# Optimization experiments

Hardware: AMD Instinct MI355X
Metric: run time of the kernel (lower is better)

Reference implementation:

```python
import jax, jax.numpy as jnp
import numpy as np

B, T, S = 32, 200, 256          # batch, decoder steps, encoder (memory) length
L = 512                          # latent_dims
U = 2 * L                        # LSTM units / attention units / attention_layer_size
E = 512                          # encoder memory feature dim
M = 80                           # mel_bins


def setup_inputs() -> dict:
    key = jax.random.key(0)
    ks = jax.random.split(key, 16)
    s = 0.05
    inputs = jax.random.normal(ks[0], (B, T, M), jnp.float32)
    memory = jax.random.normal(ks[1], (B, S, E), jnp.float32)
    # pre-net: Dense(2L, relu) -> Dropout -> Dense(L, relu) -> Dropout
    W1 = jax.random.normal(ks[2], (M, 2 * L), jnp.float32) * s
    b1 = jnp.zeros((2 * L,), jnp.float32)
    W2 = jax.random.normal(ks[3], (2 * L, L), jnp.float32) * s
    b2 = jnp.zeros((L,), jnp.float32)
    # LSTMCell(2L): input = concat(prenet_out [L], attention [U=2L]) -> 3L
    Wx = jax.random.normal(ks[4], (3 * L, 4 * U), jnp.float32) * s
    Wh = jax.random.normal(ks[5], (U, 4 * U), jnp.float32) * s
    b_lstm = jnp.zeros((4 * U,), jnp.float32)
    # Bahdanau attention (units=U): memory_layer, query_layer (no bias), score vector v
    Wm = jax.random.normal(ks[6], (E, U), jnp.float32) * s
    Wq = jax.random.normal(ks[7], (U, U), jnp.float32) * s
    v_att = jax.random.normal(ks[8], (U,), jnp.float32) * s
    # attention_layer (Dense, no bias): concat(cell_output [U], context [E]) -> U
    Wa = jax.random.normal(ks[9], (U + E, U), jnp.float32) * s
    # output projection to mel bins
    Wp = jax.random.normal(ks[10], (U, M), jnp.float32) * s
    bp = jnp.zeros((M,), jnp.float32)
    return dict(inputs=inputs, memory=memory, W1=W1, b1=b1, W2=W2, b2=b2,
                Wx=Wx, Wh=Wh, b_lstm=b_lstm, Wm=Wm, Wq=Wq, v_att=v_att,
                Wa=Wa, Wp=Wp, bp=bp)


def reference(inputs, memory, W1, b1, W2, b2, Wx, Wh, b_lstm, Wm, Wq, v_att, Wa, Wp, bp):
    # pre-net (inference: dropout is identity)
    x = jax.nn.relu(inputs @ W1 + b1)
    x = jax.nn.relu(x @ W2 + b2)                       # [B,T,L]
    keys = memory @ Wm                                 # precomputed attention keys [B,S,U]

    def step(carry, xt):
        h, c, attn = carry
        cell_in = jnp.concatenate([xt, attn], axis=-1)  # [B, 3L]
        z = cell_in @ Wx + h @ Wh + b_lstm              # [B, 4U]
        i, f, g, o = jnp.split(z, 4, axis=-1)
        c_new = jax.nn.sigmoid(f) * c + jax.nn.sigmoid(i) * jnp.tanh(g)
        h_new = jax.nn.sigmoid(o) * jnp.tanh(c_new)
        # Bahdanau additive attention
        q = h_new @ Wq                                  # [B,U]
        score = jnp.einsum('u,bsu->bs', v_att, jnp.tanh(keys + q[:, None, :]))
        align = jax.nn.softmax(score, axis=-1)          # [B,S]
        ctx = jnp.einsum('bs,bse->be', align, memory)   # [B,E]
        attn_new = jnp.concatenate([h_new, ctx], axis=-1) @ Wa  # [B,U]
        return (h_new, c_new, attn_new), attn_new

    init = (jnp.zeros((B, U), x.dtype), jnp.zeros((B, U), x.dtype), jnp.zeros((B, U), x.dtype))
    xs = jnp.swapaxes(x, 0, 1)                          # [T,B,L]
    (h, c, attn), ys = jax.lax.scan(step, init, xs)
    outs = jnp.swapaxes(ys, 0, 1)                       # [B,T,U]
    mel = outs @ Wp + bp                                # [B,T,M]
    return (mel, h, c, attn)
```

## Files before the change

### kernel.cpp

```cpp
#include <hip/hip_runtime.h>


typedef unsigned short us16;
typedef unsigned int u32;
typedef unsigned long long u64;
typedef __attribute__((ext_vector_type(8))) short bf16x8;
typedef __attribute__((ext_vector_type(4))) float f32x4;

#define MFMA16 __builtin_amdgcn_mfma_f32_16x16x32_bf16
#define AGT __HIP_MEMORY_SCOPE_AGENT

__device__ __forceinline__ us16 f2bf(float f){
  u32 u = __builtin_bit_cast(u32, f);
  u += 0x7fffu + ((u >> 16) & 1u);
  return (us16)(u >> 16);
}
__device__ __forceinline__ float bf2f(us16 h){
  return __builtin_bit_cast(float, ((u32)h) << 16);
}
__device__ __forceinline__ float h2f(us16 u){
  _Float16 h = __builtin_bit_cast(_Float16, u); return (float)h;
}
__device__ __forceinline__ us16 f2h(float f){
  _Float16 h = (_Float16)f; return __builtin_bit_cast(us16, h);
}
__device__ __forceinline__ void split3(float v, us16& s0, us16& s1, us16& s2){
  s0 = f2bf(v); float r = v - bf2f(s0);
  s1 = f2bf(r); r -= bf2f(s1);
  s2 = f2bf(r);
}
__device__ __forceinline__ float tanh_fast(float x){
  float e = __expf(-2.f * fmaxf(x, -40.f));
  return (1.f - e) / (1.f + e);
}
__device__ __forceinline__ float sigf(float x){
  return 1.f / (1.f + __expf(-x));
}

__device__ __forceinline__ u32 aload32(const u32* p){
  return __hip_atomic_load(p, __ATOMIC_RELAXED, AGT);
}
__device__ __forceinline__ void astore16(us16* p, us16 v){
  __hip_atomic_store(p, v, __ATOMIC_RELAXED, AGT);
}
__device__ __forceinline__ void astoref(float* p, float v){
  __hip_atomic_store(p, v, __ATOMIC_RELAXED, AGT);
}
__device__ __forceinline__ void sigflag(u32* p, u32 v){
  __hip_atomic_store(p, v, __ATOMIC_RELAXED, AGT);
}
__device__ __forceinline__ void aaddf(float* p, float v){
  __hip_atomic_fetch_add(p, v, __ATOMIC_RELAXED, AGT);
}
__device__ __forceinline__ bf16x8 ld16(const us16* p){
  return *(const bf16x8*)p;
}
__device__ __forceinline__ bf16x8 pin_reg(bf16x8 v){
  f32x4 t = __builtin_bit_cast(f32x4, v);
  asm volatile("" : "+v"(t));
  return __builtin_bit_cast(bf16x8, t);
}
__device__ __forceinline__ void f32_frag3(const float* p, float rs,
                                          bf16x8& f0, bf16x8& f1, bf16x8& f2){
  float4 t0 = *(const float4*)p;
  float4 t1 = *(const float4*)(p + 4);
  float tf[8] = {t0.x, t0.y, t0.z, t0.w, t1.x, t1.y, t1.z, t1.w};
#pragma unroll
  for (int i = 0; i < 8; ++i){
    float v = tf[i] * rs;
    us16 s0, s1, s2; split3(v, s0, s1, s2);
    f0[i] = (short)s0; f1[i] = (short)s1; f2[i] = (short)s2;
  }
}

#define OFF_WTA    0ull
#define OFF_WQT    50331648ull
#define OFF_X2P    56623104ull
#define OFF_KEYH   76283904ull
#define OFF_KEYL   93061120ull
#define OFF_X1     76283904ull
#define OFF_HPR    129597440ull
#define OFF_UCR    169115648ull
#define OFF_SR     182288384ull
#define OFF_CB     182314112ull
#define OFF_HF     182445184ull
#define OFF_WAPN   182576256ull
#define OFF_BPERM  182822016ull
#define OFF_ARR    182838400ull
#define OFF_QR     182870016ull
#define TOTAL_WS   209094656ull

#define WTPL 8388608ull
#define WQPL 1048576ull
#define X2PL 3276800ull

#define SA0 0
#define SA1 1
#define SB0 2
#define SB1 3
#define SC0 4
#define SC1 5

__global__ void k_init(u32* hpr0, float* ucr, float* sr, float* cbuf, u32* arr,
                       const float* __restrict__ bl, float* __restrict__ bpm){
  u32 id = blockIdx.x * 256u + threadIdx.x;
  const u32 gs = 65536u;
  for (u32 i = id; i < 49152u;   i += gs) hpr0[i] = 0u;
  for (u32 i = id; i < 3293184u; i += gs) ucr[i]  = 0.f;
  for (u32 i = id; i < 6432u;    i += gs) sr[i]   = (i < 32u) ? 1.f : 0.f;
  for (u32 i = id; i < 32768u;   i += gs) cbuf[i] = 0.f;
  for (u32 i = id; i < 2048u;    i += gs) arr[i]  = 0u;
  if (id < 4096u) bpm[((id & 1023u) << 2) | (id >> 10)] = bl[id];
}

__global__ void k_transp3(const float* __restrict__ src, us16* __restrict__ dst,
                          int srows, int scols, int ldd, long long pstride, int perm){
  __shared__ float tile[32][33];
  int bx = blockIdx.x * 32, by = blockIdx.y * 32;
  int tx = threadIdx.x & 31, ty = threadIdx.x >> 5;
#pragma unroll
  for (int i = 0; i < 4; ++i){
    int r = by + ty + i * 8, c = bx + tx;
    tile[ty + i * 8][tx] = (r < srows && c < scols) ? src[(size_t)r * scols + c] : 0.f;
  }
  __syncthreads();
#pragma unroll
  for (int i = 0; i < 4; ++i){
    int c = bx + ty + i * 8;
    int r = by + tx;
    if (c < scols && r < srows){
      int oc = perm ? (((c & 1023) << 2) | (c >> 10)) : c;
      float v = tile[tx][ty + i * 8];
      us16 s0, s1, s2; split3(v, s0, s1, s2);
      size_t base = (size_t)oc * ldd + r;
      dst[base] = s0; dst[(size_t)pstride + base] = s1; dst[2ull * pstride + base] = s2;
    }
  }
}

template<int NP, int AF, int BF>
__global__ void __launch_bounds__(256)
k_gemm3(const void* __restrict__ Ap, const void* __restrict__ Bp, void* __restrict__ outp,
        int M, int N, int K, int mode, const float* __restrict__ aux, int ldd){
  __shared__ us16 At[NP][128][72];
  __shared__ us16 Bt[NP][64][72];
  const int tid = threadIdx.x, wv = tid >> 6, lane = tid & 63;
  const int r0 = lane & 15, kg = lane >> 4;
  const int rb = blockIdx.x * 128, cb = blockIdx.y * 64;
  f32x4 acc[2][4];
#pragma unroll
  for (int a = 0; a < 2; ++a)
#pragma unroll
    for (int b = 0; b < 4; ++b) acc[a][b] = (f32x4){0.f, 0.f, 0.f, 0.f};

  const int nkt = (K + 63) >> 6;
  for (int kt = 0; kt < nkt; ++kt){
    const int kb = kt * 64;
    for (int e = tid; e < 8192; e += 256){
      int r = e >> 6, k = e & 63, ga = rb + r, gk = kb + k;
      bool ok = (ga < M) && (gk < K);
      if constexpr (AF == 1){
        float v = ok ? ((const float*)Ap)[(size_t)ga * K + gk] : 0.f;
        us16 s0, s1, s2; split3(v, s0, s1, s2);
        At[0][r][k] = s0;
        if constexpr (NP == 3){ At[1][r][k] = s1; At[2][r][k] = s2; }
      } else {
        At[0][r][k] = ok ? ((const us16*)Ap)[(size_t)ga * K + gk] : (us16)0;
      }
    }
    for (int e = tid; e < 4096; e += 256){
      int kr = e >> 6, c = e & 63, gk = kb + kr, gc = cb + c;
      bool ok = (gk < K) && (gc < N);
      if constexpr (BF == 1){
        float v = ok ? ((const float*)Bp)[(size_t)gk * N + gc] : 0.f;
        us16 s0, s1, s2; split3(v, s0, s1, s2);
        Bt[0][c][kr] = s0;
        if constexpr (NP == 3){ Bt[1][c][kr] = s1; Bt[2][c][kr] = s2; }
      } else {
        Bt[0][c][kr] = ok ? ((const us16*)Bp)[(size_t)gk * N + gc] : (us16)0;
      }
    }
    __syncthreads();
#pragma unroll
    for (int kk = 0; kk < 64; kk += 32){
      bf16x8 af[NP][2];
#pragma unroll
      for (int p = 0; p < NP; ++p){
        af[p][0] = *(const bf16x8*)&At[p][wv * 32 + r0][kk + kg * 8];
        af[p][1] = *(const bf16x8*)&At[p][wv * 32 + 16 + r0][kk + kg * 8];
      }
#pragma unroll
      for (int cf = 0; cf < 4; ++cf){
        bf16x8 bv[NP];
#pragma unroll
        for (int p = 0; p < NP; ++p) bv[p] = *(const bf16x8*)&Bt[p][cf * 16 + r0][kk + kg * 8];
#pragma unroll
        for (int rf = 0; rf < 2; ++rf){
          acc[rf][cf] = MFMA16(af[0][rf], bv[0], acc[rf][cf], 0, 0, 0);
          if constexpr (NP == 3){
            acc[rf][cf] = MFMA16(af[0][rf], bv[1], acc[rf][cf], 0, 0, 0);
            acc[rf][cf] = MFMA16(af[1][rf], bv[0], acc[rf][cf], 0, 0, 0);
            acc[rf][cf] = MFMA16(af[0][rf], bv[2], acc[rf][cf], 0, 0, 0);
            acc[rf][cf] = MFMA16(af[1][rf], bv[1], acc[rf][cf], 0, 0, 0);
            acc[rf][cf] = MFMA16(af[2][rf], bv[0], acc[rf][cf], 0, 0, 0);
          }
        }
      }
    }
    __syncthreads();
  }
  us16* o16 = (us16*)outp; float* of = (float*)outp;
#pragma unroll
  for (int rf = 0; rf < 2; ++rf)
#pragma unroll
    for (int cf = 0; cf < 4; ++cf)
#pragma unroll
      for (int i = 0; i < 4; ++i){
        int r = rb + wv * 32 + rf * 16 + kg * 4 + i;
        int c = cb + cf * 16 + r0;
        if (r >= M || c >= N) continue;
        float v = acc[rf][cf][i];
        if (mode == 0){
          of[(size_t)r * ldd + c] = fmaxf(v + aux[c], 0.f);
        } else if (mode == 1){
          v = fmaxf(v + aux[c], 0.f);
          us16 s0, s1, s2; split3(v, s0, s1, s2);
          size_t b2 = (size_t)r * ldd + c;
          o16[b2] = s0; o16[X2PL + b2] = s1; o16[2 * X2PL + b2] = s2;
        } else if (mode == 2){
          us16 hh = f2h(v); float rem = v - h2f(hh); us16 hl = f2h(rem);
          size_t b2 = (size_t)r * 1024 + c;
          o16[b2] = hh; o16[WTPL + b2] = hl;
        } else if (mode == 3){
          float w = v + (r < 1024 ? aux[(size_t)r * 4096 + c] : 0.f);
          int pc = (c & 1023) * 4 + (c >> 10);
          us16 s0, s1, s2; split3(w, s0, s1, s2);
          size_t b2 = (size_t)pc * 2048 + 512 + r;
          o16[b2] = s0; o16[WTPL + b2] = s1; o16[2 * WTPL + b2] = s2;
        } else {
          o16[(size_t)r * ldd + c] = f2bf(v);
        }
      }
}

template<int BF>
__global__ void __launch_bounds__(256)
k_gemmE(const us16* __restrict__ hpr, const float* __restrict__ ucr,
        const float* __restrict__ sr, const void* __restrict__ Bp,
        float* __restrict__ of, int M, int N, int K, int mode,
        const float* __restrict__ aux, int ldd, int ro){
  __shared__ us16 At[128][72];
  __shared__ us16 Bt[64][72];
  const int tid = threadIdx.x, wv = tid >> 6, lane = tid & 63;
  const int r0 = lane & 15, kg = lane >> 4;
  const int rb = blockIdx.x * 128, cb = blockIdx.y * 64;
  f32x4 acc[2][4];
#pragma unroll
  for (int a = 0; a < 2; ++a)
#pragma unroll
    for (int b = 0; b < 4; ++b) acc[a][b] = (f32x4){0.f, 0.f, 0.f, 0.f};

  const int nkt = (K + 63) >> 6;
  for (int kt = 0; kt < nkt; ++kt){
    const int kb = kt * 64;
    for (int e = tid; e < 8192; e += 256){
      int r = e >> 6, k = e & 63, ga = rb + r, gk = kb + k;
      us16 v = 0;
      if (ga < M && gk < K){
        int row = ro + ga, t = row >> 5, b = row & 31;
        if (gk < 1024){
          v = hpr[(size_t)t * 98304 + b * 1024 + gk];
        } else {
          float rs = 1.f / sr[(size_t)t * 32 + b];
          v = f2bf(ucr[(size_t)t * 16384 + b * 512 + (gk - 1024)] * rs);
        }
      }
      At[r][k] = v;
    }
    for (int e = tid; e < 4096; e += 256){
      int kr = e >> 6, c = e & 63, gk = kb + kr, gc = cb + c;
      bool ok = (gk < K) && (gc < N);
      if constexpr (BF == 1){
        float v = ok ? ((const float*)Bp)[(size_t)gk * N + gc] : 0.f;
        Bt[c][kr] = f2bf(v);
      } else {
        Bt[c][kr] = ok ? ((const us16*)Bp)[(size_t)gk * N + gc] : (us16)0;
      }
    }
    __syncthreads();
#pragma unroll
    for (int kk = 0; kk < 64; kk += 32){
      bf16x8 a0 = *(const bf16x8*)&At[wv * 32 + r0][kk + kg * 8];
      bf16x8 a1 = *(const bf16x8*)&At[wv * 32 + 16 + r0][kk + kg * 8];
#pragma unroll
      for (int cf = 0; cf < 4; ++cf){
        bf16x8 bv = *(const bf16x8*)&Bt[cf * 16 + r0][kk + kg * 8];
        acc[0][cf] = MFMA16(a0, bv, acc[0][cf], 0, 0, 0);
        acc[1][cf] = MFMA16(a1, bv, acc[1][cf], 0, 0, 0);
      }
    }
    __syncthreads();
  }
#pragma unroll
  for (int rf = 0; rf < 2; ++rf)
#pragma unroll
    for (int cf = 0; cf < 4; ++cf)
#pragma unroll
      for (int i = 0; i < 4; ++i){
        int r = rb + wv * 32 + rf * 16 + kg * 4 + i;
        int c = cb + cf * 16 + r0;
        if (r >= M || c >= N) continue;
        float v = acc[rf][cf][i];
        if (mode == 5){
          of[((size_t)(r & 31) * 200 + (r >> 5)) * 80 + c] = v + aux[c];
        } else {
          of[(size_t)r * ldd + c] = v;
        }
      }
}

__device__ __forceinline__ void arrv(u32* arr, int set, u32 ng, u32 ep, int tid, int blk){
  __syncthreads();
  if (tid == 0){
    int g = (blk >> 5) & 7;
    u32 old = __hip_atomic_fetch_add(&arr[(set * 8 + g) * 32], 1u, __ATOMIC_RELAXED, AGT);
    if (old == 32u * ep - 1u){
      u32 r = __hip_atomic_fetch_add(&arr[(48 + set) * 32], 1u, __ATOMIC_RELAXED, AGT);
      if (r == ng * ep - 1u)
        sigflag(&arr[(56 + set) * 32], ep);
    }
  }
}
__device__ __forceinline__ void waitrel(u32* arr, int set, u32 ep, int tid){
  if (tid == 0){
    while (aload32(&arr[(56 + set) * 32]) < ep) __builtin_amdgcn_s_sleep(2);
    __builtin_amdgcn_sched_barrier(0);
  }
  __syncthreads();
}

struct CoopA {
  const us16 *wta, *wqt, *x2p, *kh, *kl;
  const float *mem, *vatt, *bperm;
  us16 *hpr;
  float *ucr, *sr, *qr, *cbuf, *hf32;
  u32 *arr;
};

__global__ void __launch_bounds__(512, 1) k_coop(CoopA a){
  __shared__ us16 khi[32][1024];
  __shared__ us16 klo[32][1024];
  __shared__ float zp[8][512];
  __shared__ float esc[16];

  __builtin_amdgcn_fence(__ATOMIC_ACQUIRE, "agent");

  const int tid = threadIdx.x, blk = blockIdx.x;
  const int wv = tid >> 6, lane = tid & 63;
  const int r0 = lane & 15, kg = lane >> 4;
  const int b16 = blk >> 4, s0c = (blk & 15) * 16;
  const int colbase = blk * 16;
  const int u0 = lane * 16;

  bf16x8 wr[8][3];
#pragma unroll
  for (int ks = 0; ks < 8; ++ks){
    const size_t wb = (size_t)(colbase + r0) * 2048 + (size_t)wv * 256 + ks * 32 + kg * 8;
#pragma unroll
    for (int p = 0; p < 3; ++p)
      wr[ks][p] = pin_reg(*(const bf16x8*)&a.wta[(size_t)p * WTPL + wb]);
  }

  {
    for (int i = tid; i < 4096; i += 512){
      int r = i >> 7, c8 = (i & 127) * 8;
      int gb = (r < 16) ? b16 : (16 + b16);
      int s  = s0c + (r & 15);
      const size_t kb = ((size_t)(gb * 256 + s)) * 1024 + c8;
      *(bf16x8*)&khi[r][c8] = *(const bf16x8*)&a.kh[kb];
      *(bf16x8*)&klo[r][c8] = *(const bf16x8*)&a.kl[kb];
    }
  }
  __syncthreads();

  auto phaseA = [&](int g, int t){
    const int gr = g * 16;
    f32x4 acc = (f32x4){0.f, 0.f, 0.f, 0.f};
    float rsv = (wv >= 6) ? 1.f / a.sr[(size_t)t * 32 + gr + r0] : 0.f;
#pragma unroll
    for (int ks = 0; ks < 8; ++ks){
      const int kf = wv * 256 + ks * 32 + kg * 8;
      bf16x8 w0 = wr[ks][0], w1 = wr[ks][1], w2 = wr[ks][2];
      bf16x8 a0, a1, a2;
      if (wv < 2){
        const size_t xb = ((size_t)(gr + r0) * 200 + t) * 512 + kf;
        a0 = *(const bf16x8*)&a.x2p[xb];
        a1 = *(const bf16x8*)&a.x2p[X2PL + xb];
        a2 = *(const bf16x8*)&a.x2p[2 * X2PL + xb];
      } else if (wv < 6){
        const int hk = kf - 512;
        const us16* hb = a.hpr + (size_t)t * 98304 + (size_t)(gr + r0) * 1024 + hk;
        a0 = ld16(hb); a1 = ld16(hb + 32768); a2 = ld16(hb + 65536);
      } else {
        const int ek = kf - 1536;
        const float* up = a.ucr + (size_t)t * 16384 + (size_t)(gr + r0) * 512 + ek;
        f32_frag3(up, rsv, a0, a1, a2);
      }
      acc = MFMA16(a0, w0, acc, 0,0,0); acc = MFMA16(a0, w1, acc, 0,0,0);
      acc = MFMA16(a1, w0, acc, 0,0,0); acc = MFMA16(a0, w2, acc, 0,0,0);
      acc = MFMA16(a1, w1, acc, 0,0,0); acc = MFMA16(a2, w0, acc, 0,0,0);
    }
#pragma unroll
    for (int i = 0; i < 4; ++i)
      zp[wv][(kg * 4 + i) * 16 + r0] = acc[i];
    __syncthreads();
    float z = 0.f;
    if (tid < 256){
#pragma unroll
      for (int w = 0; w < 8; ++w) z += zp[w][tid];
      z += a.bperm[colbase + (tid & 15)];
    }
    __syncthreads();
    if (tid < 256) zp[0][tid] = z;
    __syncthreads();
    if (tid < 64){
      int bl = tid >> 2, ul = tid & 3, u = blk * 4 + ul;
      int b = gr + bl;
      float zi = zp[0][bl * 16 + ul * 4 + 0];
      float zf = zp[0][bl * 16 + ul * 4 + 1];
      float zg = zp[0][bl * 16 + ul * 4 + 2];
      float zo = zp[0][bl * 16 + ul * 4 + 3];
      float co = a.cbuf[b * 1024 + u];
      float cn = sigf(zf) * co + sigf(zi) * tanh_fast(zg);
      float hn = sigf(zo) * tanh_fast(cn);
      a.cbuf[b * 1024 + u] = cn;
      a.hf32[b * 1024 + u] = hn;
      us16 s0, s1, s2; split3(hn, s0, s1, s2);
      us16* hb = a.hpr + (size_t)(t + 1) * 98304 + b * 1024 + u;
      astore16(hb, s0);
      astore16(hb + 32768, s1);
      astore16(hb + 65536, s2);
    }
  };

  auto phaseB = [&](int g, int t, int colb){
    const int gr = g * 16;
    f32x4 acc = (f32x4){0.f, 0.f, 0.f, 0.f};
#pragma unroll
    for (int ks = 0; ks < 4; ++ks){
      const int kf = wv * 128 + ks * 32 + kg * 8;
      const size_t wb = (size_t)(colb + r0) * 1024 + kf;
      bf16x8 w0 = *(const bf16x8*)&a.wqt[wb];
      bf16x8 w1 = *(const bf16x8*)&a.wqt[WQPL + wb];
      bf16x8 w2 = *(const bf16x8*)&a.wqt[2 * WQPL + wb];
      const us16* hb = a.hpr + (size_t)(t + 1) * 98304 + (size_t)(gr + r0) * 1024 + kf;
      bf16x8 a0 = ld16(hb), a1 = ld16(hb + 32768), a2 = ld16(hb + 65536);
      acc = MFMA16(a0, w0, acc, 0,0,0); acc = MFMA16(a0, w1, acc, 0,0,0);
      acc = MFMA16(a1, w0, acc, 0,0,0); acc = MFMA16(a0, w2, acc, 0,0,0);
      acc = MFMA16(a1, w1, acc, 0,0,0); acc = MFMA16(a2, w0, acc, 0,0,0);
    }
#pragma unroll
    for (int i = 0; i < 4; ++i)
      zp[wv][(kg * 4 + i) * 16 + r0] = acc[i];
    __syncthreads();
    if (tid < 256){
      float q = 0.f;
#pragma unroll
      for (int w = 0; w < 8; ++w) q += zp[w][tid];
      astoref(&a.qr[(size_t)t * 32768 + (size_t)(gr + (tid >> 4)) * 1024 + colb + (tid & 15)], q);
    }
  };

  auto phaseC = [&](int g, int t){
    const int b = g * 16 + b16;
    float qv[16], vv[16];
    {
      const float* qp = a.qr + (size_t)t * 32768 + (size_t)b * 1024 + u0;
      float4 q0 = *(const float4*)qp;
      float4 q1 = *(const float4*)(qp + 4);
      float4 q2 = *(const float4*)(qp + 8);
      float4 q3 = *(const float4*)(qp + 12);
      qv[0]=q0.x; qv[1]=q0.y; qv[2]=q0.z; qv[3]=q0.w;
      qv[4]=q1.x; qv[5]=q1.y; qv[6]=q1.z; qv[7]=q1.w;
      qv[8]=q2.x; qv[9]=q2.y; qv[10]=q2.z; qv[11]=q2.w;
      qv[12]=q3.x; qv[13]=q3.y; qv[14]=q3.z; qv[15]=q3.w;
      float4 v0 = *(const float4*)(a.vatt + u0);
      float4 v1 = *(const float4*)(a.vatt + u0 + 4);
      float4 v2 = *(const float4*)(a.vatt + u0 + 8);
      float4 v3 = *(const float4*)(a.vatt + u0 + 12);
      vv[0]=v0.x; vv[1]=v0.y; vv[2]=v0.z; vv[3]=v0.w;
      vv[4]=v1.x; vv[5]=v1.y; vv[6]=v1.z; vv[7]=v1.w;
      vv[8]=v2.x; vv[9]=v2.y; vv[10]=v2.z; vv[11]=v2.w;
      vv[12]=v3.x; vv[13]=v3.y; vv[14]=v3.z; vv[15]=v3.w;
    }
#pragma unroll
    for (int m = 0; m < 2; ++m){
      const int sl = wv * 2 + m;
      const int kr = g * 16 + sl;
      bf16x8 h0 = *(const bf16x8*)&khi[kr][u0];
      bf16x8 h1 = *(const bf16x8*)&khi[kr][u0 + 8];
      bf16x8 l0 = *(const bf16x8*)&klo[kr][u0];
      bf16x8 l1 = *(const bf16x8*)&klo[kr][u0 + 8];
      float part = 0.f;
#pragma unroll
      for (int j = 0; j < 8; ++j){
        float kva = h2f((us16)h0[j]) + h2f((us16)l0[j]);
        part += vv[j] * tanh_fast(kva + qv[j]);
        float kvb = h2f((us16)h1[j]) + h2f((us16)l1[j]);
        part += vv[8 + j] * tanh_fast(kvb + qv[8 + j]);
      }
#pragma unroll
      for (int off = 32; off; off >>= 1) part += __shfl_xor(part, off);
      if (lane == 0) esc[sl] = __expf(part);
    }
    __syncthreads();
    if (tid == 0){
      float bs = 0.f;
#pragma unroll
      for (int i = 0; i < 16; ++i) bs += esc[i];
      aaddf(&a.sr[(size_t)(t + 1) * 32 + b], bs);
    }
    {
      float ac0 = 0.f, ac1 = 0.f;
      const float* mrow = a.mem + ((size_t)(b * 256 + s0c)) * 512 + tid;
#pragma unroll
      for (int j = 0; j < 16; j += 2){
        ac0 += esc[j]     * mrow[(size_t)j * 512];
        ac1 += esc[j + 1] * mrow[(size_t)(j + 1) * 512];
      }
      aaddf(&a.ucr[(size_t)(t + 1) * 16384 + b * 512 + tid], ac0 + ac1);
    }
    __syncthreads();
  };

  for (int t = 0; t < 200; ++t){
    const u32 ep = (u32)(t + 1);
    waitrel(a.arr, SC0, (u32)t, tid);
    phaseA(0, t);
    arrv(a.arr, SA0, 8, ep, tid, blk);
    waitrel(a.arr, SC1, (u32)t, tid);
    phaseA(1, t);
    arrv(a.arr, SA1, 8, ep, tid, blk);
    if (blk < 64){
      waitrel(a.arr, SA0, ep, tid);
      phaseB(0, t, blk * 16);
      arrv(a.arr, SB0, 2, ep, tid, blk);
    } else if (blk < 128){
      waitrel(a.arr, SA1, ep, tid);
      phaseB(1, t, (blk - 64) * 16);
      arrv(a.arr, SB1, 2, ep, tid, blk);
    }
    waitrel(a.arr, SB0, ep, tid);
    phaseC(0, t);
    arrv(a.arr, SC0, 8, ep, tid, blk);
    waitrel(a.arr, SB1, ep, tid);
    phaseC(1, t);
    arrv(a.arr, SC1, 8, ep, tid, blk);
  }
}

__global__ void k_copy_hc(const float* __restrict__ h, const float* __restrict__ c,
                          float* __restrict__ out){
  int i = blockIdx.x * 256 + threadIdx.x;
  if (i < 32768){
    out[512000 + i] = h[i];
    out[544768 + i] = c[i];
  }
}

extern "C" void kernel_launch(void* const* d_in, const int* in_sizes, int n_in,
                              void* d_out, int out_size, void* d_ws, size_t ws_size,
                              hipStream_t stream){
  const float* inputs = (const float*)d_in[0];
  const float* memory = (const float*)d_in[1];
  const float* W1     = (const float*)d_in[2];
  const float* b1     = (const float*)d_in[3];
  const float* W2     = (const float*)d_in[4];
  const float* b2     = (const float*)d_in[5];
  const float* Wx     = (const float*)d_in[6];
  const float* Wh     = (const float*)d_in[7];
  const float* b_lstm = (const float*)d_in[8];
  const float* Wm     = (const float*)d_in[9];
  const float* Wq     = (const float*)d_in[10];
  const float* v_att  = (const float*)d_in[11];
  const float* Wa     = (const float*)d_in[12];
  const float* Wp     = (const float*)d_in[13];
  const float* bp     = (const float*)d_in[14];
  float* out = (float*)d_out;
  char* ws = (char*)d_ws;
  if (ws_size < TOTAL_WS) return;

  us16* WTA    = (us16*)(ws + OFF_WTA);
  us16* WQT    = (us16*)(ws + OFF_WQT);
  us16* X2P    = (us16*)(ws + OFF_X2P);
  us16* KEYH   = (us16*)(ws + OFF_KEYH);
  float* X1    = (float*)(ws + OFF_X1);
  us16* HPR    = (us16*)(ws + OFF_HPR);
  float* UCR   = (float*)(ws + OFF_UCR);
  float* SR    = (float*)(ws + OFF_SR);
  float* QR    = (float*)(ws + OFF_QR);
  float* CB    = (float*)(ws + OFF_CB);
  float* HF    = (float*)(ws + OFF_HF);
  us16* WAPN   = (us16*)(ws + OFF_WAPN);
  float* BPM   = (float*)(ws + OFF_BPERM);
  u32*  ARR    = (u32*)(ws + OFF_ARR);

  k_init<<<256, 256, 0, stream>>>((u32*)HPR, UCR, SR, CB, ARR, b_lstm, BPM);
  k_transp3<<<dim3(32, 32), 256, 0, stream>>>(Wq, WQT, 1024, 1024, 1024, (long long)WQPL, 0);
  k_transp3<<<dim3(128, 16), 256, 0, stream>>>(Wx, WTA, 512, 4096, 2048, (long long)WTPL, 1);

  k_gemm3<3,1,1><<<dim3(12, 64), 256, 0, stream>>>(Wa, Wx + (size_t)512 * 4096, WTA,
                                                   1536, 4096, 1024, 3, Wh, 0);
  k_gemm3<3,1,1><<<dim3(12, 2), 256, 0, stream>>>(Wa, Wp, WAPN, 1536, 80, 1024, 4, nullptr, 80);
  k_gemm3<3,1,1><<<dim3(50, 16), 256, 0, stream>>>(inputs, W1, X1, 6400, 1024, 80, 0, b1, 1024);
  k_gemm3<3,1,1><<<dim3(50, 8), 256, 0, stream>>>(X1, W2, X2P, 6400, 512, 1024, 1, b2, 512);
  k_gemm3<3,1,1><<<dim3(64, 16), 256, 0, stream>>>(memory, Wm, KEYH, 8192, 1024, 512, 2, nullptr, 1024);

  CoopA ca;
  ca.wta = WTA; ca.wqt = WQT; ca.x2p = X2P; ca.kh = KEYH; ca.kl = KEYH + WTPL;
  ca.mem = memory; ca.vatt = v_att; ca.bperm = BPM;
  ca.hpr = HPR; ca.ucr = UCR; ca.sr = SR;
  ca.qr = QR; ca.cbuf = CB; ca.hf32 = HF; ca.arr = ARR;
  void* args[] = {(void*)&ca};
  hipLaunchCooperativeKernel((const void*)k_coop, dim3(256), dim3(512), args, 0, stream);

  k_gemmE<0><<<dim3(50, 2), 256, 0, stream>>>(HPR, UCR, SR, WAPN, out,
                                              6400, 80, 1536, 5, bp, 0, 32);
  k_gemmE<1><<<dim3(1, 16), 256, 0, stream>>>(HPR, UCR, SR, Wa, out + 577536,
                                              32, 1024, 1536, 6, nullptr, 1024, 6400);
  k_copy_hc<<<128, 256, 0, stream>>>(HF, CB, out);
}
```

Baseline: 11.69 ms.

## Fuse prologue and epilogue launches into merged kernels with wider GEMM tiles

```diff
diff --git a/kernel.cpp b/kernel.cpp
--- a/kernel.cpp
+++ b/kernel.cpp
@@ -78,7 +78,6 @@
 #define OFF_X2P    56623104ull
 #define OFF_KEYH   76283904ull
 #define OFF_KEYL   93061120ull
-#define OFF_X1     76283904ull
 #define OFF_HPR    129597440ull
 #define OFF_UCR    169115648ull
 #define OFF_SR     182288384ull
@@ -101,57 +100,20 @@
 #define SC0 4
 #define SC1 5
 
-__global__ void k_init(u32* hpr0, float* ucr, float* sr, float* cbuf, u32* arr,
-                       const float* __restrict__ bl, float* __restrict__ bpm){
-  u32 id = blockIdx.x * 256u + threadIdx.x;
-  const u32 gs = 65536u;
-  for (u32 i = id; i < 49152u;   i += gs) hpr0[i] = 0u;
-  for (u32 i = id; i < 3293184u; i += gs) ucr[i]  = 0.f;
-  for (u32 i = id; i < 6432u;    i += gs) sr[i]   = (i < 32u) ? 1.f : 0.f;
-  for (u32 i = id; i < 32768u;   i += gs) cbuf[i] = 0.f;
-  for (u32 i = id; i < 2048u;    i += gs) arr[i]  = 0u;
-  if (id < 4096u) bpm[((id & 1023u) << 2) | (id >> 10)] = bl[id];
-}
-
-__global__ void k_transp3(const float* __restrict__ src, us16* __restrict__ dst,
-                          int srows, int scols, int ldd, long long pstride, int perm){
-  __shared__ float tile[32][33];
-  int bx = blockIdx.x * 32, by = blockIdx.y * 32;
-  int tx = threadIdx.x & 31, ty = threadIdx.x >> 5;
-#pragma unroll
-  for (int i = 0; i < 4; ++i){
-    int r = by + ty + i * 8, c = bx + tx;
-    tile[ty + i * 8][tx] = (r < srows && c < scols) ? src[(size_t)r * scols + c] : 0.f;
-  }
-  __syncthreads();
-#pragma unroll
-  for (int i = 0; i < 4; ++i){
-    int c = bx + ty + i * 8;
-    int r = by + tx;
-    if (c < scols && r < srows){
-      int oc = perm ? (((c & 1023) << 2) | (c >> 10)) : c;
-      float v = tile[tx][ty + i * 8];
-      us16 s0, s1, s2; split3(v, s0, s1, s2);
-      size_t base = (size_t)oc * ldd + r;
-      dst[base] = s0; dst[(size_t)pstride + base] = s1; dst[2ull * pstride + base] = s2;
-    }
-  }
-}
-
-template<int NP, int AF, int BF>
-__global__ void __launch_bounds__(256)
-k_gemm3(const void* __restrict__ Ap, const void* __restrict__ Bp, void* __restrict__ outp,
-        int M, int N, int K, int mode, const float* __restrict__ aux, int ldd){
-  __shared__ us16 At[NP][128][72];
-  __shared__ us16 Bt[NP][64][72];
+__device__ void gemm3_dev(char* smem, int bx, int by,
+                          const float* __restrict__ Ap, const float* __restrict__ Bp,
+                          void* __restrict__ outp, int M, int N, int K, int mode,
+                          const float* __restrict__ aux, int ldd){
+  us16* At = (us16*)smem;
+  us16* Bt = (us16*)(smem + 55296);
   const int tid = threadIdx.x, wv = tid >> 6, lane = tid & 63;
   const int r0 = lane & 15, kg = lane >> 4;
-  const int rb = blockIdx.x * 128, cb = blockIdx.y * 64;
-  f32x4 acc[2][4];
+  const int rb = bx * 128, cb = by * 128;
+  f32x4 acc[2][8];
 #pragma unroll
   for (int a = 0; a < 2; ++a)
 #pragma unroll
-    for (int b = 0; b < 4; ++b) acc[a][b] = (f32x4){0.f, 0.f, 0.f, 0.f};
+    for (int b = 0; b < 8; ++b) acc[a][b] = (f32x4){0.f, 0.f, 0.f, 0.f};
 
   const int nkt = (K + 63) >> 6;
   for (int kt = 0; kt < nkt; ++kt){
@@ -159,51 +121,44 @@
     for (int e = tid; e < 8192; e += 256){
       int r = e >> 6, k = e & 63, ga = rb + r, gk = kb + k;
       bool ok = (ga < M) && (gk < K);
-      if constexpr (AF == 1){
-        float v = ok ? ((const float*)Ap)[(size_t)ga * K + gk] : 0.f;
-        us16 s0, s1, s2; split3(v, s0, s1, s2);
-        At[0][r][k] = s0;
-        if constexpr (NP == 3){ At[1][r][k] = s1; At[2][r][k] = s2; }
-      } else {
-        At[0][r][k] = ok ? ((const us16*)Ap)[(size_t)ga * K + gk] : (us16)0;
-      }
-    }
-    for (int e = tid; e < 4096; e += 256){
-      int kr = e >> 6, c = e & 63, gk = kb + kr, gc = cb + c;
+      float v = ok ? Ap[(size_t)ga * K + gk] : 0.f;
+      us16 s0, s1, s2; split3(v, s0, s1, s2);
+      At[r * 72 + k] = s0;
+      At[(128 + r) * 72 + k] = s1;
+      At[(256 + r) * 72 + k] = s2;
+    }
+    for (int e = tid; e < 8192; e += 256){
+      int kr = e >> 7, c = e & 127, gk = kb + kr, gc = cb + c;
       bool ok = (gk < K) && (gc < N);
-      if constexpr (BF == 1){
-        float v = ok ? ((const float*)Bp)[(size_t)gk * N + gc] : 0.f;
-        us16 s0, s1, s2; split3(v, s0, s1, s2);
-        Bt[0][c][kr] = s0;
-        if constexpr (NP == 3){ Bt[1][c][kr] = s1; Bt[2][c][kr] = s2; }
-      } else {
-        Bt[0][c][kr] = ok ? ((const us16*)Bp)[(size_t)gk * N + gc] : (us16)0;
-      }
+      float v = ok ? Bp[(size_t)gk * N + gc] : 0.f;
+      us16 s0, s1, s2; split3(v, s0, s1, s2);
+      Bt[c * 72 + kr] = s0;
+      Bt[(128 + c) * 72 + kr] = s1;
+      Bt[(256 + c) * 72 + kr] = s2;
     }
     __syncthreads();
 #pragma unroll
     for (int kk = 0; kk < 64; kk += 32){
-      bf16x8 af[NP][2];
-#pragma unroll
-      for (int p = 0; p < NP; ++p){
-        af[p][0] = *(const bf16x8*)&At[p][wv * 32 + r0][kk + kg * 8];
-        af[p][1] = *(const bf16x8*)&At[p][wv * 32 + 16 + r0][kk + kg * 8];
-      }
-#pragma unroll
-      for (int cf = 0; cf < 4; ++cf){
-        bf16x8 bv[NP];
-#pragma unroll
-        for (int p = 0; p < NP; ++p) bv[p] = *(const bf16x8*)&Bt[p][cf * 16 + r0][kk + kg * 8];
+      bf16x8 af[3][2];
+#pragma unroll
+      for (int p = 0; p < 3; ++p){
+        af[p][0] = *(const bf16x8*)&At[(p * 128 + wv * 32 + r0) * 72 + kk + kg * 8];
+        af[p][1] = *(const bf16x8*)&At[(p * 128 + wv * 32 + 16 + r0) * 72 + kk + kg * 8];
+      }
+#pragma unroll
+      for (int cf = 0; cf < 8; ++cf){
+        bf16x8 bv[3];
+#pragma unroll
+        for (int p = 0; p < 3; ++p)
+          bv[p] = *(const bf16x8*)&Bt[(p * 128 + cf * 16 + r0) * 72 + kk + kg * 8];
 #pragma unroll
         for (int rf = 0; rf < 2; ++rf){
           acc[rf][cf] = MFMA16(af[0][rf], bv[0], acc[rf][cf], 0, 0, 0);
-          if constexpr (NP == 3){
-            acc[rf][cf] = MFMA16(af[0][rf], bv[1], acc[rf][cf], 0, 0, 0);
-            acc[rf][cf] = MFMA16(af[1][rf], bv[0], acc[rf][cf], 0, 0, 0);
-            acc[rf][cf] = MFMA16(af[0][rf], bv[2], acc[rf][cf], 0, 0, 0);
-            acc[rf][cf] = MFMA16(af[1][rf], bv[1], acc[rf][cf], 0, 0, 0);
-            acc[rf][cf] = MFMA16(af[2][rf], bv[0], acc[rf][cf], 0, 0, 0);
-          }
+          acc[rf][cf] = MFMA16(af[0][rf], bv[1], acc[rf][cf], 0, 0, 0);
+          acc[rf][cf] = MFMA16(af[1][rf], bv[0], acc[rf][cf], 0, 0, 0);
+          acc[rf][cf] = MFMA16(af[0][rf], bv[2], acc[rf][cf], 0, 0, 0);
+          acc[rf][cf] = MFMA16(af[1][rf], bv[1], acc[rf][cf], 0, 0, 0);
+          acc[rf][cf] = MFMA16(af[2][rf], bv[0], acc[rf][cf], 0, 0, 0);
         }
       }
     }
@@ -213,7 +168,7 @@
 #pragma unroll
   for (int rf = 0; rf < 2; ++rf)
 #pragma unroll
-    for (int cf = 0; cf < 4; ++cf)
+    for (int cf = 0; cf < 8; ++cf)
 #pragma unroll
       for (int i = 0; i < 4; ++i){
         int r = rb + wv * 32 + rf * 16 + kg * 4 + i;
@@ -243,17 +198,88 @@
       }
 }
 
-template<int BF>
-__global__ void __launch_bounds__(256)
-k_gemmE(const us16* __restrict__ hpr, const float* __restrict__ ucr,
-        const float* __restrict__ sr, const void* __restrict__ Bp,
-        float* __restrict__ of, int M, int N, int K, int mode,
-        const float* __restrict__ aux, int ldd, int ro){
-  __shared__ us16 At[128][72];
-  __shared__ us16 Bt[64][72];
+__device__ void transp3_dev(char* smem, int bxi, int byi,
+                            const float* __restrict__ src, us16* __restrict__ dst,
+                            int srows, int scols, int ldd, long long pstride, int perm){
+  float (*tile)[33] = (float(*)[33])smem;
+  int bx = bxi * 32, by = byi * 32;
+  int tx = threadIdx.x & 31, ty = threadIdx.x >> 5;
+#pragma unroll
+  for (int i = 0; i < 4; ++i){
+    int r = by + ty + i * 8, c = bx + tx;
+    tile[ty + i * 8][tx] = (r < srows && c < scols) ? src[(size_t)r * scols + c] : 0.f;
+  }
+  __syncthreads();
+#pragma unroll
+  for (int i = 0; i < 4; ++i){
+    int c = bx + ty + i * 8;
+    int r = by + tx;
+    if (c < scols && r < srows){
+      int oc = perm ? (((c & 1023) << 2) | (c >> 10)) : c;
+      float v = tile[tx][ty + i * 8];
+      us16 s0, s1, s2; split3(v, s0, s1, s2);
+      size_t base = (size_t)oc * ldd + r;
+      dst[base] = s0; dst[(size_t)pstride + base] = s1; dst[2ull * pstride + base] = s2;
+    }
+  }
+}
+
+struct MegaA {
+  const float *inputs, *mem, *W1, *b1, *Wx, *Wh, *bl, *Wm, *Wq, *Wa, *Wp;
+  us16 *WTA, *WQT, *KEYH, *WAPN;
+  float *X1, *bpm;
+  u32 *hpr0; float *ucr, *sr, *cbuf; u32 *arr;
+};
+
+__global__ void __launch_bounds__(256) k_mega(MegaA m){
+  __shared__ __align__(16) char smem[110592];
+  const int blk = blockIdx.x;
+  if (blk < 384){
+    gemm3_dev(smem, blk % 12, blk / 12, m.Wa, m.Wx + (size_t)512 * 4096,
+              m.WTA, 1536, 4096, 1024, 3, m.Wh, 0);
+  } else if (blk < 396){
+    gemm3_dev(smem, blk - 384, 0, m.Wa, m.Wp, m.WAPN, 1536, 80, 1024, 4, nullptr, 80);
+  } else if (blk < 796){
+    int b = blk - 396;
+    gemm3_dev(smem, b % 50, b / 50, m.inputs, m.W1, m.X1, 6400, 1024, 80, 0, m.b1, 1024);
+  } else if (blk < 1308){
+    int b = blk - 796;
+    gemm3_dev(smem, b % 64, b / 64, m.mem, m.Wm, m.KEYH, 8192, 1024, 512, 2, nullptr, 1024);
+  } else if (blk < 2332){
+    int b = blk - 1308;
+    transp3_dev(smem, b % 32, b / 32, m.Wq, m.WQT, 1024, 1024, 1024, (long long)WQPL, 0);
+  } else if (blk < 4380){
+    int b = blk - 2332;
+    transp3_dev(smem, b % 128, b / 128, m.Wx, m.WTA, 512, 4096, 2048, (long long)WTPL, 1);
+  } else {
+    u32 id = (u32)(blk - 4380) * 256u + threadIdx.x;
+    const u32 gs = 65536u;
+    for (u32 i = id; i < 49152u;   i += gs) m.hpr0[i] = 0u;
+    for (u32 i = id; i < 3293184u; i += gs) m.ucr[i]  = 0.f;
+    for (u32 i = id; i < 6432u;    i += gs) m.sr[i]   = (i < 32u) ? 1.f : 0.f;
+    for (u32 i = id; i < 32768u;   i += gs) m.cbuf[i] = 0.f;
+    for (u32 i = id; i < 2048u;    i += gs) m.arr[i]  = 0u;
+    if (id < 4096u) m.bpm[((id & 1023u) << 2) | (id >> 10)] = m.bl[id];
+  }
+}
+
+struct P2A { const float *X1, *W2, *b2; us16* X2P; };
+__global__ void __launch_bounds__(256) k_p2(P2A p){
+  __shared__ __align__(16) char smem[110592];
+  gemm3_dev(smem, blockIdx.x % 50, blockIdx.x / 50, p.X1, p.W2, p.X2P,
+            6400, 512, 1024, 1, p.b2, 512);
+}
+
+__device__ void gemmE_dev(char* smem, int bx, int by, int BF,
+                          const us16* __restrict__ hpr, const float* __restrict__ ucr,
+                          const float* __restrict__ sr, const void* __restrict__ Bp,
+                          float* __restrict__ of, int M, int N, int K, int mode,
+                          const float* __restrict__ aux, int ldd, int ro){
+  us16* At = (us16*)smem;
+  us16* Bt = (us16*)(smem + 18432);
   const int tid = threadIdx.x, wv = tid >> 6, lane = tid & 63;
   const int r0 = lane & 15, kg = lane >> 4;
-  const int rb = blockIdx.x * 128, cb = blockIdx.y * 64;
+  const int rb = bx * 128, cb = by * 64;
   f32x4 acc[2][4];
 #pragma unroll
   for (int a = 0; a < 2; ++a)
@@ -275,26 +301,26 @@
           v = f2bf(ucr[(size_t)t * 16384 + b * 512 + (gk - 1024)] * rs);
         }
       }
-      At[r][k] = v;
+      At[r * 72 + k] = v;
     }
     for (int e = tid; e < 4096; e += 256){
       int kr = e >> 6, c = e & 63, gk = kb + kr, gc = cb + c;
       bool ok = (gk < K) && (gc < N);
-      if constexpr (BF == 1){
+      if (BF == 1){
         float v = ok ? ((const float*)Bp)[(size_t)gk * N + gc] : 0.f;
-        Bt[c][kr] = f2bf(v);
+        Bt[c * 72 + kr] = f2bf(v);
       } else {
-        Bt[c][kr] = ok ? ((const us16*)Bp)[(size_t)gk * N + gc] : (us16)0;
+        Bt[c * 72 + kr] = ok ? ((const us16*)Bp)[(size_t)gk * N + gc] : (us16)0;
       }
     }
     __syncthreads();
 #pragma unroll
     for (int kk = 0; kk < 64; kk += 32){
-      bf16x8 a0 = *(const bf16x8*)&At[wv * 32 + r0][kk + kg * 8];
-      bf16x8 a1 = *(const bf16x8*)&At[wv * 32 + 16 + r0][kk + kg * 8];
+      bf16x8 a0 = *(const bf16x8*)&At[(wv * 32 + r0) * 72 + kk + kg * 8];
+      bf16x8 a1 = *(const bf16x8*)&At[(wv * 32 + 16 + r0) * 72 + kk + kg * 8];
 #pragma unroll
       for (int cf = 0; cf < 4; ++cf){
-        bf16x8 bv = *(const bf16x8*)&Bt[cf * 16 + r0][kk + kg * 8];
+        bf16x8 bv = *(const bf16x8*)&Bt[(cf * 16 + r0) * 72 + kk + kg * 8];
         acc[0][cf] = MFMA16(a0, bv, acc[0][cf], 0, 0, 0);
         acc[1][cf] = MFMA16(a1, bv, acc[1][cf], 0, 0, 0);
       }
@@ -317,6 +343,29 @@
           of[(size_t)r * ldd + c] = v;
         }
       }
+}
+
+struct EpiA {
+  const us16 *hpr; const float *ucr, *sr;
+  const us16 *WAPN; const float *Wa, *bp, *hf, *cb;
+  float *out;
+};
+__global__ void __launch_bounds__(256) k_epi(EpiA e){
+  __shared__ __align__(16) char smem[27648];
+  const int blk = blockIdx.x;
+  if (blk < 100){
+    gemmE_dev(smem, blk % 50, blk / 50, 0, e.hpr, e.ucr, e.sr, e.WAPN,
+              e.out, 6400, 80, 1536, 5, e.bp, 0, 32);
+  } else if (blk < 116){
+    gemmE_dev(smem, 0, blk - 100, 1, e.hpr, e.ucr, e.sr, e.Wa,
+              e.out + 577536, 32, 1024, 1536, 6, nullptr, 1024, 6400);
+  } else {
+    int i = (blk - 116) * 256 + threadIdx.x;
+    if (i < 32768){
+      e.out[512000 + i] = e.hf[i];
+      e.out[544768 + i] = e.cb[i];
+    }
+  }
 }
 
 __device__ __forceinline__ void arrv(u32* arr, int set, u32 ng, u32 ep, int tid, int blk){
@@ -559,15 +608,6 @@
   }
 }
 
-__global__ void k_copy_hc(const float* __restrict__ h, const float* __restrict__ c,
-                          float* __restrict__ out){
-  int i = blockIdx.x * 256 + threadIdx.x;
-  if (i < 32768){
-    out[512000 + i] = h[i];
-    out[544768 + i] = c[i];
-  }
-}
-
 extern "C" void kernel_launch(void* const* d_in, const int* in_sizes, int n_in,
                               void* d_out, int out_size, void* d_ws, size_t ws_size,
                               hipStream_t stream){
@@ -594,27 +634,27 @@
   us16* WQT    = (us16*)(ws + OFF_WQT);
   us16* X2P    = (us16*)(ws + OFF_X2P);
   us16* KEYH   = (us16*)(ws + OFF_KEYH);
-  float* X1    = (float*)(ws + OFF_X1);
   us16* HPR    = (us16*)(ws + OFF_HPR);
   float* UCR   = (float*)(ws + OFF_UCR);
   float* SR    = (float*)(ws + OFF_SR);
   float* QR    = (float*)(ws + OFF_QR);
+  float* X1    = (float*)(ws + OFF_QR);
   float* CB    = (float*)(ws + OFF_CB);
   float* HF    = (float*)(ws + OFF_HF);
   us16* WAPN   = (us16*)(ws + OFF_WAPN);
   float* BPM   = (float*)(ws + OFF_BPERM);
   u32*  ARR    = (u32*)(ws + OFF_ARR);
 
-  k_init<<<256, 256, 0, stream>>>((u32*)HPR, UCR, SR, CB, ARR, b_lstm, BPM);
-  k_transp3<<<dim3(32, 32), 256, 0, stream>>>(Wq, WQT, 1024, 1024, 1024, (long long)WQPL, 0);
-  k_transp3<<<dim3(128, 16), 256, 0, stream>>>(Wx, WTA, 512, 4096, 2048, (long long)WTPL, 1);
-
-  k_gemm3<3,1,1><<<dim3(12, 64), 256, 0, stream>>>(Wa, Wx + (size_t)512 * 4096, WTA,
-                                                   1536, 4096, 1024, 3, Wh, 0);
-  k_gemm3<3,1,1><<<dim3(12, 2), 256, 0, stream>>>(Wa, Wp, WAPN, 1536, 80, 1024, 4, nullptr, 80);
-  k_gemm3<3,1,1><<<dim3(50, 16), 256, 0, stream>>>(inputs, W1, X1, 6400, 1024, 80, 0, b1, 1024);
-  k_gemm3<3,1,1><<<dim3(50, 8), 256, 0, stream>>>(X1, W2, X2P, 6400, 512, 1024, 1, b2, 512);
-  k_gemm3<3,1,1><<<dim3(64, 16), 256, 0, stream>>>(memory, Wm, KEYH, 8192, 1024, 512, 2, nullptr, 1024);
+  MegaA ma;
+  ma.inputs = inputs; ma.mem = memory; ma.W1 = W1; ma.b1 = b1; ma.Wx = Wx;
+  ma.Wh = Wh; ma.bl = b_lstm; ma.Wm = Wm; ma.Wq = Wq; ma.Wa = Wa; ma.Wp = Wp;
+  ma.WTA = WTA; ma.WQT = WQT; ma.KEYH = KEYH; ma.WAPN = WAPN;
+  ma.X1 = X1; ma.bpm = BPM;
+  ma.hpr0 = (u32*)HPR; ma.ucr = UCR; ma.sr = SR; ma.cbuf = CB; ma.arr = ARR;
+  k_mega<<<4636, 256, 0, stream>>>(ma);
+
+  P2A p2; p2.X1 = X1; p2.W2 = W2; p2.b2 = b2; p2.X2P = X2P;
+  k_p2<<<200, 256, 0, stream>>>(p2);
 
   CoopA ca;
   ca.wta = WTA; ca.wqt = WQT; ca.x2p = X2P; ca.kh = KEYH; ca.kl = KEYH + WTPL;
@@ -624,9 +664,8 @@
   void* args[] = {(void*)&ca};
   hipLaunchCooperativeKernel((const void*)k_coop, dim3(256), dim3(512), args, 0, stream);
 
-  k_gemmE<0><<<dim3(50, 2), 256, 0, stream>>>(HPR, UCR, SR, WAPN, out,
-                                              6400, 80, 1536, 5, bp, 0, 32);
-  k_gemmE<1><<<dim3(1, 16), 256, 0, stream>>>(HPR, UCR, SR, Wa, out + 577536,
-                                              32, 1024, 1536, 6, nullptr, 1024, 6400);
-  k_copy_hc<<<128, 256, 0, stream>>>(HF, CB, out);
-}
+  EpiA ea;
+  ea.hpr = HPR; ea.ucr = UCR; ea.sr = SR; ea.WAPN = WAPN; ea.Wa = Wa;
+  ea.bp = bp; ea.hf = HF; ea.cb = CB; ea.out = out;
+  k_epi<<<244, 256, 0, stream>>>(ea);
+}
```

Result: faster. 10.59 ms (-9.4%).
